# Performance work log

Measured on AMD Instinct MI355X. Metric: run time of the kernel, lower is better.

## Reference

```python
import jax, jax.numpy as jnp
import numpy as np

FILTERS = 512
DQK = FILTERS // 8  # 64


def setup_inputs() -> dict:
    key = jax.random.key(0)
    ks = jax.random.split(key, 7)
    B, H, W, C = 32, 32, 32, FILTERS
    x = jax.random.normal(ks[0], (B, H, W, C), dtype=jnp.float32)
    # 1x1 convs == per-pixel dense layers: weight [Cin, Cout], bias [Cout]
    def glorot(k, cin, cout):
        lim = np.sqrt(6.0 / (cin + cout)).astype(np.float32)
        return jax.random.uniform(k, (cin, cout), jnp.float32, -lim, lim)
    return {
        "x": x,
        "wq": glorot(ks[1], C, DQK), "bq": jnp.zeros((DQK,), jnp.float32),
        "wk": glorot(ks[2], C, DQK), "bk": jnp.zeros((DQK,), jnp.float32),
        "wv": glorot(ks[3], C, C),   "bv": jnp.zeros((C,), jnp.float32),
    }


def reference(x, wq, bq, wk, bk, wv, bv):
    B, H, W, C = x.shape
    N = H * W
    xf = x.reshape(B, N, C)                       # flatten spatial -> tokens
    q = xf @ wq + bq                              # [B, N, C//8]
    k = xf @ wk + bk                              # [B, N, C//8]
    v = xf @ wv + bv                              # [B, N, C]
    scale = 1.0 / jnp.sqrt(jnp.float32(C // 8))
    scores = jnp.einsum('bnd,bmd->bnm', q, k) * scale  # [B, N, N]
    probs = jax.nn.softmax(scores, axis=-1)
    attended = jnp.einsum('bnm,bmc->bnc', probs, v)    # [B, N, C]
    return attended.reshape(B, H, W, C) + x
```

## Files before the change

### kernel.cpp

```cpp
#include <hip/hip_runtime.h>
#include <stdint.h>

#define B_ 32
#define N_ 1024
#define C_ 512
#define D_ 64

typedef __attribute__((ext_vector_type(8))) __bf16 bf8;
typedef __attribute__((ext_vector_type(4))) float f32x4;

typedef const __attribute__((address_space(1))) void* gp_t;
typedef __attribute__((address_space(3))) void* lp_t;

__device__ inline void g2l16(const void* g, void* l) {
    __builtin_amdgcn_global_load_lds((gp_t)g, (lp_t)l, 16, 0, 0);
}

__device__ inline float b2f(unsigned short u) {
    return __uint_as_float(((unsigned)u) << 16);
}
__device__ inline unsigned short f2b(float f) {
    unsigned u = __float_as_uint(f);
    u += 0x7FFF + ((u >> 16) & 1);
    return (unsigned short)(u >> 16);
}

#define MFMA16(a, b, c) __builtin_amdgcn_mfma_f32_16x16x32_bf16((a), (b), (c), 0, 0, 0)

__device__ __forceinline__ void ld_frags(const unsigned short* As, const unsigned short* Bs,
                                         int wm, int wn, int lane,
                                         bf8 (&a)[2][4], bf8 (&bb)[2][4]) {
    #pragma unroll
    for (int kq = 0; kq < 2; ++kq) {
        #pragma unroll
        for (int ti = 0; ti < 4; ++ti)
            a[kq][ti] = *(const bf8*)&As[((wm * 4 + ti) * 2 + kq) * 512 + lane * 8];
        #pragma unroll
        for (int tj = 0; tj < 4; ++tj)
            bb[kq][tj] = *(const bf8*)&Bs[((wn * 4 + tj) * 2 + kq) * 512 + lane * 8];
    }
}

__device__ __forceinline__ void do_mfma(const bf8 (&a)[2][4], const bf8 (&bb)[2][4],
                                        f32x4 (&acc)[4][4]) {
    #pragma unroll
    for (int kq = 0; kq < 2; ++kq)
        #pragma unroll
        for (int ti = 0; ti < 4; ++ti)
            #pragma unroll
            for (int tj = 0; tj < 4; ++tj)
                acc[ti][tj] = MFMA16(a[kq][ti], bb[kq][tj], acc[ti][tj]);
}

__global__ __launch_bounds__(256) void xcvt(const float* __restrict__ x,
                                            unsigned short* __restrict__ xb) {
    int i = blockIdx.x * 256 + threadIdx.x;
    float4 f = ((const float4*)x)[i];
    ushort4 o;
    o.x = f2b(f.x); o.y = f2b(f.y); o.z = f2b(f.z); o.w = f2b(f.w);
    ((ushort4*)xb)[i] = o;
}

__global__ __launch_bounds__(256) void wtrans_all(
    const float* __restrict__ wq, const float* __restrict__ wk,
    const float* __restrict__ wv, unsigned short* __restrict__ wt)
{
    int t = blockIdx.x * 256 + threadIdx.x;
    int co = t >> 9;
    int ci = t & 511;
    const float* src;
    int col, cout;
    if (co < 64)       { src = wq; col = co;       cout = 64;  }
    else if (co < 128) { src = wk; col = co - 64;  cout = 64;  }
    else               { src = wv; col = co - 128; cout = 512; }
    wt[t] = f2b(src[(size_t)ci * cout + col]);
}

__global__ __launch_bounds__(256) void qkv(
    const unsigned short* __restrict__ xb,
    const unsigned short* __restrict__ WT,
    const float* __restrict__ bq, const float* __restrict__ bk,
    const float* __restrict__ bv,
    unsigned short* __restrict__ q, unsigned short* __restrict__ k,
    unsigned short* __restrict__ vT)
{
    const int rb = blockIdx.x;
    const int cb = blockIdx.y;
    const int tid = threadIdx.x;
    const int lane = tid & 63;
    const int wave = tid >> 6;
    const int wm = wave >> 1, wn = wave & 1;
    const int lr = lane & 15;
    const int lk = lane >> 4;

    __shared__ unsigned short SM[32768];
    unsigned short* TB = SM;

    const int row0 = rb * 128;
    const int col0 = cb * 128;

    f32x4 zero4 = {0.f, 0.f, 0.f, 0.f};
    f32x4 acc[4][4];
    #pragma unroll
    for (int i = 0; i < 4; ++i)
        #pragma unroll
        for (int j = 0; j < 4; ++j) acc[i][j] = zero4;

    auto stage = [&](int buf, int kk) {
        unsigned short* As = SM + buf * 8192;
        unsigned short* Bs = SM + 16384 + buf * 8192;
        #pragma unroll
        for (int i = 0; i < 4; ++i) {
            int f = wave * 4 + i;
            int t = f >> 1, kq = f & 1;
            g2l16(xb + (size_t)(row0 + t * 16 + lr) * C_ + kk + kq * 32 + lk * 8,
                  &As[f * 512]);
            g2l16(WT + (size_t)(col0 + t * 16 + lr) * C_ + kk + kq * 32 + lk * 8,
                  &Bs[f * 512]);
        }
    };

    stage(0, 0);
    stage(1, 64);
    int cur = 0;
    for (int t = 0; t < 6; ++t) {
        asm volatile("s_waitcnt vmcnt(8)" ::: "memory");
        __builtin_amdgcn_s_barrier();
        bf8 a[2][4], bb[2][4];
        ld_frags(SM + cur * 8192, SM + 16384 + cur * 8192, wm, wn, lane, a, bb);
        asm volatile("s_waitcnt lgkmcnt(0)" ::: "memory");
        __builtin_amdgcn_s_barrier();
        stage(cur, (t + 2) * 64);
        do_mfma(a, bb, acc);
        cur ^= 1;
    }
    {
        asm volatile("s_waitcnt vmcnt(8)" ::: "memory");
        __builtin_amdgcn_s_barrier();
        bf8 a[2][4], bb[2][4];
        ld_frags(SM + cur * 8192, SM + 16384 + cur * 8192, wm, wn, lane, a, bb);
        do_mfma(a, bb, acc);
        cur ^= 1;
    }
    {
        asm volatile("s_waitcnt vmcnt(0)" ::: "memory");
        __builtin_amdgcn_s_barrier();
        bf8 a[2][4], bb[2][4];
        ld_frags(SM + cur * 8192, SM + 16384 + cur * 8192, wm, wn, lane, a, bb);
        do_mfma(a, bb, acc);
    }

    if (cb == 0) {
        unsigned short* outp = (wn == 0) ? q : k;
        const float* bias = (wn == 0) ? bq : bk;
        #pragma unroll
        for (int ti = 0; ti < 4; ++ti)
            #pragma unroll
            for (int tj = 0; tj < 4; ++tj) {
                int col = tj * 16 + lr;
                float bi = bias[col];
                #pragma unroll
                for (int r = 0; r < 4; ++r) {
                    int row = row0 + wm * 64 + ti * 16 + lk * 4 + r;
                    outp[(size_t)row * D_ + col] = f2b(acc[ti][tj][r] + bi);
                }
            }
    } else {
        const int colv = (cb - 1) * 128;
        __syncthreads();
        #pragma unroll
        for (int ti = 0; ti < 4; ++ti)
            #pragma unroll
            for (int tj = 0; tj < 4; ++tj) {
                int c = wn * 64 + tj * 16 + lr;
                float bi = bv[colv + c];
                int tok = wm * 64 + ti * 16 + lk * 4;
                ushort4 o;
                o.x = f2b(acc[ti][tj][0] + bi);
                o.y = f2b(acc[ti][tj][1] + bi);
                o.z = f2b(acc[ti][tj][2] + bi);
                o.w = f2b(acc[ti][tj][3] + bi);
                *(ushort4*)&TB[c * 132 + tok] = o;
            }
        __syncthreads();
        const int b  = row0 >> 10;
        const int n0 = row0 & 1023;
        #pragma unroll
        for (int i = 0; i < 16; ++i) {
            int idx = tid + 256 * i;
            int c = idx >> 5, ch = idx & 31;
            ushort4 t4 = *(const ushort4*)&TB[c * 132 + ch * 4];
            *(ushort4*)&vT[((size_t)(b * C_ + colv + c)) * N_ + n0 + ch * 4] = t4;
        }
    }
}

#define SLD 1032
__global__ __launch_bounds__(256) void scores(
    const unsigned short* __restrict__ q,
    const unsigned short* __restrict__ k,
    unsigned short* __restrict__ P)
{
    const int qt = blockIdx.x, b = blockIdx.y;
    const int tid = threadIdx.x, lane = tid & 63, wave = tid >> 6;
    const int lr = lane & 15, lk = lane >> 4;
    __shared__ unsigned short S[16 * SLD];

    const int n0 = qt * 16;
    const unsigned short* qrow = q + (size_t)(b * N_ + n0 + lr) * D_ + lk * 8;
    bf8 qa0 = *(const bf8*)(qrow);
    bf8 qa1 = *(const bf8*)(qrow + 32);

    const int m0w = wave * 256;
    #pragma unroll 4
    for (int mt = 0; mt < 16; ++mt) {
        int m = m0w + mt * 16;
        const unsigned short* krow = k + (size_t)(b * N_ + m + lr) * D_ + lk * 8;
        bf8 kb0 = *(const bf8*)(krow);
        bf8 kb1 = *(const bf8*)(krow + 32);
        f32x4 s = {0.f, 0.f, 0.f, 0.f};
        s = MFMA16(qa0, kb0, s);
        s = MFMA16(qa1, kb1, s);
        #pragma unroll
        for (int r = 0; r < 4; ++r)
            S[(lk * 4 + r) * SLD + m + lr] = f2b(s[r] * 0.125f);
    }
    __syncthreads();

    #pragma unroll
    for (int rr4 = 0; rr4 < 4; ++rr4) {
        int rr = wave * 4 + rr4;
        float vals[16];
        float mx = -1e30f;
        #pragma unroll
        for (int j = 0; j < 16; ++j) {
            vals[j] = b2f(S[rr * SLD + j * 64 + lane]);
            mx = fmaxf(mx, vals[j]);
        }
        #pragma unroll
        for (int off = 32; off; off >>= 1) mx = fmaxf(mx, __shfl_xor(mx, off));
        float sum = 0.f;
        #pragma unroll
        for (int j = 0; j < 16; ++j) { vals[j] = __expf(vals[j] - mx); sum += vals[j]; }
        #pragma unroll
        for (int off = 32; off; off >>= 1) sum += __shfl_xor(sum, off);
        float inv = 1.f / sum;
        unsigned short* pp = P + (size_t)(b * N_ + n0 + rr) * N_;
        #pragma unroll
        for (int j = 0; j < 16; ++j) pp[j * 64 + lane] = f2b(vals[j] * inv);
    }
}

__global__ __launch_bounds__(256) void pv(
    const unsigned short* __restrict__ P,
    const unsigned short* __restrict__ vT,
    const float* __restrict__ x,
    float* __restrict__ out)
{
    const int m0 = blockIdx.x * 128, c0 = blockIdx.y * 128, b = blockIdx.z;
    const int tid = threadIdx.x, lane = tid & 63, wave = tid >> 6;
    const int wm = wave >> 1, wn = wave & 1;
    const int lr = lane & 15, lk = lane >> 4;

    __shared__ unsigned short As[2][8192];
    __shared__ unsigned short Bs[2][8192];

    f32x4 zero4 = {0.f, 0.f, 0.f, 0.f};
    f32x4 acc[4][4];
    #pragma unroll
    for (int i = 0; i < 4; ++i)
        #pragma unroll
        for (int j = 0; j < 4; ++j) acc[i][j] = zero4;

    const unsigned short* Pb = P  + (size_t)b * N_ * N_;
    const unsigned short* Vb = vT + (size_t)b * C_ * N_;

    auto stage = [&](int buf, int kk) {
        #pragma unroll
        for (int i = 0; i < 4; ++i) {
            int f = wave * 4 + i;
            int t = f >> 1, kq = f & 1;
            g2l16(Pb + (size_t)(m0 + t * 16 + lr) * N_ + kk + kq * 32 + lk * 8,
                  &As[buf][f * 512]);
            g2l16(Vb + (size_t)(c0 + t * 16 + lr) * N_ + kk + kq * 32 + lk * 8,
                  &Bs[buf][f * 512]);
        }
    };

    stage(0, 0);
    stage(1, 64);
    int cur = 0;
    for (int t = 0; t < 14; ++t) {
        asm volatile("s_waitcnt vmcnt(8)" ::: "memory");
        __builtin_amdgcn_s_barrier();
        bf8 a[2][4], bb[2][4];
        ld_frags(&As[cur][0], &Bs[cur][0], wm, wn, lane, a, bb);
        asm volatile("s_waitcnt lgkmcnt(0)" ::: "memory");
        __builtin_amdgcn_s_barrier();
        stage(cur, (t + 2) * 64);
        do_mfma(a, bb, acc);
        cur ^= 1;
    }
    {
        asm volatile("s_waitcnt vmcnt(8)" ::: "memory");
        __builtin_amdgcn_s_barrier();
        bf8 a[2][4], bb[2][4];
        ld_frags(&As[cur][0], &Bs[cur][0], wm, wn, lane, a, bb);
        do_mfma(a, bb, acc);
        cur ^= 1;
    }
    {
        asm volatile("s_waitcnt vmcnt(0)" ::: "memory");
        __builtin_amdgcn_s_barrier();
        bf8 a[2][4], bb[2][4];
        ld_frags(&As[cur][0], &Bs[cur][0], wm, wn, lane, a, bb);
        do_mfma(a, bb, acc);
    }

    #pragma unroll
    for (int ti = 0; ti < 4; ++ti)
        #pragma unroll
        for (int tj = 0; tj < 4; ++tj) {
            int col = c0 + wn * 64 + tj * 16 + lr;
            #pragma unroll
            for (int r = 0; r < 4; ++r) {
                int row = m0 + wm * 64 + ti * 16 + lk * 4 + r;
                size_t idx = (size_t)(b * N_ + row) * C_ + col;
                out[idx] = acc[ti][tj][r] + x[idx];
            }
        }
}

extern "C" void kernel_launch(void* const* d_in, const int* in_sizes, int n_in,
                              void* d_out, int out_size, void* d_ws, size_t ws_size,
                              hipStream_t stream) {
    (void)in_sizes; (void)n_in; (void)out_size; (void)ws_size;
    const float* xf = (const float*)d_in[0];
    const float* wq = (const float*)d_in[1];
    const float* bq = (const float*)d_in[2];
    const float* wk = (const float*)d_in[3];
    const float* bk = (const float*)d_in[4];
    const float* wv = (const float*)d_in[5];
    const float* bv = (const float*)d_in[6];
    float* out = (float*)d_out;

    char* ws = (char*)d_ws;
    unsigned short* qb  = (unsigned short*)(ws);
    unsigned short* kb  = (unsigned short*)(ws + 4194304);
    unsigned short* vTb = (unsigned short*)(ws + 8388608);
    unsigned short* WT  = (unsigned short*)(ws + 41943040);
    unsigned short* xb  = (unsigned short*)(ws + 42598400);
    unsigned short* Pb  = (unsigned short*)(ws + 41943040);

    xcvt<<<16384, 256, 0, stream>>>(xf, xb);
    wtrans_all<<<1280, 256, 0, stream>>>(wq, wk, wv, WT);
    qkv<<<dim3(256, 5), 256, 0, stream>>>(xb, WT, bq, bk, bv, qb, kb, vTb);
    scores<<<dim3(64, 32), 256, 0, stream>>>(qb, kb, Pb);
    pv<<<dim3(8, 4, 32), 256, 0, stream>>>(Pb, vTb, xf, out);
}
```

Before: 284.4 us.

## Fuse scores, softmax and PV into one two-pass attention kernel

Replaces the separate scores/softmax kernel and PV GEMM with one fused kernel. It first makes a pass over K to compute the per-row max and sum with online rescaling, then recomputes QK^T per tile, normalizes the probabilities into LDS, and multiplies them by V tiles. This avoids writing the 32x1024x1024 bf16 probability matrix to global memory and reading it back. In exchange, QK^T is computed twice per channel block, and there are two channel blocks, and each PV step waits on a full vmcnt(0) without double-buffering V.

```diff
diff --git a/kernel.cpp b/kernel.cpp
--- a/kernel.cpp
+++ b/kernel.cpp
@@ -195,138 +195,142 @@
     }
 }
 
-#define SLD 1032
-__global__ __launch_bounds__(256) void scores(
+__global__ __launch_bounds__(256) void fused_attn(
     const unsigned short* __restrict__ q,
     const unsigned short* __restrict__ k,
-    unsigned short* __restrict__ P)
-{
-    const int qt = blockIdx.x, b = blockIdx.y;
-    const int tid = threadIdx.x, lane = tid & 63, wave = tid >> 6;
-    const int lr = lane & 15, lk = lane >> 4;
-    __shared__ unsigned short S[16 * SLD];
-
-    const int n0 = qt * 16;
-    const unsigned short* qrow = q + (size_t)(b * N_ + n0 + lr) * D_ + lk * 8;
-    bf8 qa0 = *(const bf8*)(qrow);
-    bf8 qa1 = *(const bf8*)(qrow + 32);
-
-    const int m0w = wave * 256;
-    #pragma unroll 4
-    for (int mt = 0; mt < 16; ++mt) {
-        int m = m0w + mt * 16;
-        const unsigned short* krow = k + (size_t)(b * N_ + m + lr) * D_ + lk * 8;
-        bf8 kb0 = *(const bf8*)(krow);
-        bf8 kb1 = *(const bf8*)(krow + 32);
-        f32x4 s = {0.f, 0.f, 0.f, 0.f};
-        s = MFMA16(qa0, kb0, s);
-        s = MFMA16(qa1, kb1, s);
-        #pragma unroll
-        for (int r = 0; r < 4; ++r)
-            S[(lk * 4 + r) * SLD + m + lr] = f2b(s[r] * 0.125f);
-    }
-    __syncthreads();
-
-    #pragma unroll
-    for (int rr4 = 0; rr4 < 4; ++rr4) {
-        int rr = wave * 4 + rr4;
-        float vals[16];
-        float mx = -1e30f;
-        #pragma unroll
-        for (int j = 0; j < 16; ++j) {
-            vals[j] = b2f(S[rr * SLD + j * 64 + lane]);
-            mx = fmaxf(mx, vals[j]);
-        }
-        #pragma unroll
-        for (int off = 32; off; off >>= 1) mx = fmaxf(mx, __shfl_xor(mx, off));
-        float sum = 0.f;
-        #pragma unroll
-        for (int j = 0; j < 16; ++j) { vals[j] = __expf(vals[j] - mx); sum += vals[j]; }
-        #pragma unroll
-        for (int off = 32; off; off >>= 1) sum += __shfl_xor(sum, off);
-        float inv = 1.f / sum;
-        unsigned short* pp = P + (size_t)(b * N_ + n0 + rr) * N_;
-        #pragma unroll
-        for (int j = 0; j < 16; ++j) pp[j * 64 + lane] = f2b(vals[j] * inv);
-    }
-}
-
-__global__ __launch_bounds__(256) void pv(
-    const unsigned short* __restrict__ P,
     const unsigned short* __restrict__ vT,
     const float* __restrict__ x,
     float* __restrict__ out)
 {
-    const int m0 = blockIdx.x * 128, c0 = blockIdx.y * 128, b = blockIdx.z;
+    const int qb  = blockIdx.x;
+    const int cbk = blockIdx.y;
+    const int b   = blockIdx.z;
     const int tid = threadIdx.x, lane = tid & 63, wave = tid >> 6;
-    const int wm = wave >> 1, wn = wave & 1;
     const int lr = lane & 15, lk = lane >> 4;
 
-    __shared__ unsigned short As[2][8192];
-    __shared__ unsigned short Bs[2][8192];
-
-    f32x4 zero4 = {0.f, 0.f, 0.f, 0.f};
+    __shared__ unsigned short LDS[28672];
+    unsigned short* Ps = LDS;
+    unsigned short* K0 = LDS + 4096;
+    unsigned short* K1 = LDS + 8192;
+    unsigned short* Vs = LDS + 12288;
+
+    const unsigned short* qrow =
+        q + (size_t)(b * N_ + qb * 64 + wave * 16 + lr) * D_ + lk * 8;
+    const bf8 qf0 = *(const bf8*)qrow;
+    const bf8 qf1 = *(const bf8*)(qrow + 32);
+
+    const unsigned short* Kb = k  + (size_t)b * N_ * D_;
+    const unsigned short* Vb = vT + ((size_t)b * C_ + cbk * 256) * N_;
+
+    auto stageK = [&](unsigned short* dst, int t) {
+        #pragma unroll
+        for (int i = 0; i < 2; ++i) {
+            int f = wave * 2 + i;
+            g2l16(Kb + (size_t)(t * 64 + wave * 16 + lr) * D_ + i * 32 + lk * 8,
+                  &dst[f * 512]);
+        }
+    };
+    auto stageV = [&](int t) {
+        #pragma unroll
+        for (int i = 0; i < 8; ++i) {
+            int f = wave * 8 + i;
+            int cf = f >> 1, kq = f & 1;
+            g2l16(Vb + (size_t)(cf * 16 + lr) * N_ + t * 64 + kq * 32 + lk * 8,
+                  &Vs[f * 512]);
+        }
+    };
+    auto computeS = [&](const unsigned short* K_, f32x4 (&s)[4]) {
+        #pragma unroll
+        for (int kf = 0; kf < 4; ++kf) {
+            bf8 ka0 = *(const bf8*)&K_[(kf * 2 + 0) * 512 + lane * 8];
+            bf8 ka1 = *(const bf8*)&K_[(kf * 2 + 1) * 512 + lane * 8];
+            f32x4 z = {0.f, 0.f, 0.f, 0.f};
+            z = MFMA16(ka0, qf0, z);
+            z = MFMA16(ka1, qf1, z);
+            s[kf] = z;
+        }
+    };
+
+    float m = -1e30f, l = 0.f;
+    stageK(K0, 0);
+    for (int t = 0; t < 16; ++t) {
+        asm volatile("s_waitcnt vmcnt(0)" ::: "memory");
+        __builtin_amdgcn_s_barrier();
+        if (t < 15) stageK((t & 1) ? K0 : K1, t + 1);
+        f32x4 s[4];
+        computeS((t & 1) ? K1 : K0, s);
+        float tmax = -1e30f;
+        #pragma unroll
+        for (int kf = 0; kf < 4; ++kf)
+            #pragma unroll
+            for (int r = 0; r < 4; ++r) tmax = fmaxf(tmax, s[kf][r] * 0.125f);
+        tmax = fmaxf(tmax, __shfl_xor(tmax, 16));
+        tmax = fmaxf(tmax, __shfl_xor(tmax, 32));
+        float nm = fmaxf(m, tmax);
+        float ps = 0.f;
+        #pragma unroll
+        for (int kf = 0; kf < 4; ++kf)
+            #pragma unroll
+            for (int r = 0; r < 4; ++r) ps += __expf(s[kf][r] * 0.125f - nm);
+        ps += __shfl_xor(ps, 16);
+        ps += __shfl_xor(ps, 32);
+        l = l * __expf(m - nm) + ps;
+        m = nm;
+    }
+    const float inv = 1.f / l;
+
     f32x4 acc[4][4];
     #pragma unroll
     for (int i = 0; i < 4; ++i)
         #pragma unroll
-        for (int j = 0; j < 4; ++j) acc[i][j] = zero4;
-
-    const unsigned short* Pb = P  + (size_t)b * N_ * N_;
-    const unsigned short* Vb = vT + (size_t)b * C_ * N_;
-
-    auto stage = [&](int buf, int kk) {
-        #pragma unroll
-        for (int i = 0; i < 4; ++i) {
-            int f = wave * 4 + i;
-            int t = f >> 1, kq = f & 1;
-            g2l16(Pb + (size_t)(m0 + t * 16 + lr) * N_ + kk + kq * 32 + lk * 8,
-                  &As[buf][f * 512]);
-            g2l16(Vb + (size_t)(c0 + t * 16 + lr) * N_ + kk + kq * 32 + lk * 8,
-                  &Bs[buf][f * 512]);
-        }
-    };
-
-    stage(0, 0);
-    stage(1, 64);
-    int cur = 0;
-    for (int t = 0; t < 14; ++t) {
-        asm volatile("s_waitcnt vmcnt(8)" ::: "memory");
-        __builtin_amdgcn_s_barrier();
-        bf8 a[2][4], bb[2][4];
-        ld_frags(&As[cur][0], &Bs[cur][0], wm, wn, lane, a, bb);
+        for (int j = 0; j < 4; ++j) { f32x4 z = {0.f,0.f,0.f,0.f}; acc[i][j] = z; }
+
+    stageK(K0, 0);
+    stageV(0);
+    for (int t = 0; t < 16; ++t) {
+        asm volatile("s_waitcnt vmcnt(0)" ::: "memory");
+        __builtin_amdgcn_s_barrier();
+        if (t < 15) stageK((t & 1) ? K0 : K1, t + 1);
+        f32x4 s[4];
+        computeS((t & 1) ? K1 : K0, s);
+        #pragma unroll
+        for (int kf = 0; kf < 4; ++kf) {
+            ushort4 o;
+            o.x = f2b(__expf(s[kf][0] * 0.125f - m) * inv);
+            o.y = f2b(__expf(s[kf][1] * 0.125f - m) * inv);
+            o.z = f2b(__expf(s[kf][2] * 0.125f - m) * inv);
+            o.w = f2b(__expf(s[kf][3] * 0.125f - m) * inv);
+            int f  = wave * 2 + (kf >> 1);
+            int lp = lr + 16 * ((kf & 1) * 2 + (lk >> 1));
+            *(ushort4*)&Ps[f * 512 + lp * 8 + 4 * (lk & 1)] = o;
+        }
         asm volatile("s_waitcnt lgkmcnt(0)" ::: "memory");
         __builtin_amdgcn_s_barrier();
-        stage(cur, (t + 2) * 64);
-        do_mfma(a, bb, acc);
-        cur ^= 1;
-    }
-    {
-        asm volatile("s_waitcnt vmcnt(8)" ::: "memory");
-        __builtin_amdgcn_s_barrier();
-        bf8 a[2][4], bb[2][4];
-        ld_frags(&As[cur][0], &Bs[cur][0], wm, wn, lane, a, bb);
-        do_mfma(a, bb, acc);
-        cur ^= 1;
-    }
-    {
-        asm volatile("s_waitcnt vmcnt(0)" ::: "memory");
-        __builtin_amdgcn_s_barrier();
-        bf8 a[2][4], bb[2][4];
-        ld_frags(&As[cur][0], &Bs[cur][0], wm, wn, lane, a, bb);
-        do_mfma(a, bb, acc);
-    }
-
-    #pragma unroll
-    for (int ti = 0; ti < 4; ++ti)
-        #pragma unroll
-        for (int tj = 0; tj < 4; ++tj) {
-            int col = c0 + wn * 64 + tj * 16 + lr;
+        #pragma unroll
+        for (int i = 0; i < 4; ++i)
+            #pragma unroll
+            for (int kq = 0; kq < 2; ++kq) {
+                bf8 pa = *(const bf8*)&Ps[(i * 2 + kq) * 512 + lane * 8];
+                #pragma unroll
+                for (int j = 0; j < 4; ++j) {
+                    bf8 vb = *(const bf8*)&Vs[((wave * 4 + j) * 2 + kq) * 512 + lane * 8];
+                    acc[i][j] = MFMA16(pa, vb, acc[i][j]);
+                }
+            }
+        __builtin_amdgcn_s_barrier();
+        if (t < 15) stageV(t + 1);
+    }
+
+    #pragma unroll
+    for (int i = 0; i < 4; ++i)
+        #pragma unroll
+        for (int j = 0; j < 4; ++j) {
+            int col = cbk * 256 + wave * 64 + j * 16 + lr;
             #pragma unroll
             for (int r = 0; r < 4; ++r) {
-                int row = m0 + wm * 64 + ti * 16 + lk * 4 + r;
+                int row = qb * 64 + i * 16 + lk * 4 + r;
                 size_t idx = (size_t)(b * N_ + row) * C_ + col;
-                out[idx] = acc[ti][tj][r] + x[idx];
+                out[idx] = acc[i][j][r] + x[idx];
             }
         }
 }
@@ -350,11 +354,9 @@
     unsigned short* vTb = (unsigned short*)(ws + 8388608);
     unsigned short* WT  = (unsigned short*)(ws + 41943040);
     unsigned short* xb  = (unsigned short*)(ws + 42598400);
-    unsigned short* Pb  = (unsigned short*)(ws + 41943040);
 
     xcvt<<<16384, 256, 0, stream>>>(xf, xb);
     wtrans_all<<<1280, 256, 0, stream>>>(wq, wk, wv, WT);
     qkv<<<dim3(256, 5), 256, 0, stream>>>(xb, WT, bq, bk, bv, qb, kb, vTb);
-    scores<<<dim3(64, 32), 256, 0, stream>>>(qb, kb, Pb);
-    pv<<<dim3(8, 4, 32), 256, 0, stream>>>(Pb, vTb, xf, out);
-}
+    fused_attn<<<dim3(16, 2, 32), 256, 0, stream>>>(qb, kb, vTb, xf, out);
+}
```

After: 285.8 us. About the same (+0.5%).
